# Performance work log

Hardware: AMD Instinct MI355X
Metric: run time of the kernel (lower is better)

The kernel has to match this reference:

```python
import jax, jax.numpy as jnp
import numpy as np

B, S, E, A = 4, 4096, 512, 64

def setup_inputs() -> dict:
    key = jax.random.key(0)
    ks = jax.random.split(key, 9)
    return {
        "query": jax.random.normal(ks[0], (B, S, E), dtype=jnp.float32),
        "key":   jax.random.normal(ks[1], (B, S, E), dtype=jnp.float32),
        "value": jax.random.normal(ks[2], (B, S, E), dtype=jnp.float32),
        "Wq": jax.random.normal(ks[3], (E, A), dtype=jnp.float32) / np.sqrt(E),
        "bq": jax.random.normal(ks[4], (A,), dtype=jnp.float32) * 0.01,
        "Wk": jax.random.normal(ks[5], (E, A), dtype=jnp.float32) / np.sqrt(E),
        "bk": jax.random.normal(ks[6], (A,), dtype=jnp.float32) * 0.01,
        "Wv": jax.random.normal(ks[7], (E, A), dtype=jnp.float32) / np.sqrt(E),
        "bv": jax.random.normal(ks[8], (A,), dtype=jnp.float32) * 0.01,
        "look_ahead_mask": 1,
    }

def reference(query, key, value, Wq, bq, Wk, bk, Wv, bv, look_ahead_mask):
    # Linear projections (torch Linear: x @ W^T + b; here W stored as [in,out])
    q = query @ Wq + bq            # [B,S,A]
    k = key   @ Wk + bk            # [B,S,A]
    v = value @ Wv + bv            # [B,S,A]
    scale = jnp.sqrt(jnp.asarray(A, dtype=q.dtype))
    qk = jnp.einsum('bsa,bta->bst', q, k) / scale   # [B,S,S]
    if look_ahead_mask:
        # faithful to source: MULTIPLICATIVE tril mask (not additive -inf)
        tril = jnp.tril(jnp.ones((qk.shape[-1], qk.shape[-1]), dtype=qk.dtype))
        qk = qk * tril
    attn = jax.nn.softmax(qk, axis=-1)              # [B,S,S]
    return jnp.einsum('bst,bta->bsa', attn, v)       # [B,S,A]
```

## Files before the change

### kernel.cpp

```cpp
#include <hip/hip_runtime.h>
#include <cstdint>

constexpr int BB = 4, SS = 4096, EE = 512, AA = 64;
constexpr int NT = 64;
constexpr int NSL = 288;

typedef __bf16 bf16x8 __attribute__((ext_vector_type(8)));
typedef float  f32x4  __attribute__((ext_vector_type(4)));
typedef float  f4     __attribute__((ext_vector_type(4)));
typedef unsigned short u16x4 __attribute__((ext_vector_type(4)));
typedef unsigned short u16x8 __attribute__((ext_vector_type(8)));

#define MFMA16(a, b, c) __builtin_amdgcn_mfma_f32_16x16x32_bf16((a), (b), (c), 0, 0, 0)

typedef const void __attribute__((address_space(1))) gvoid_t;
typedef void __attribute__((address_space(3))) lvoid_t;
__device__ __forceinline__ void gload16(const void* g, void* l) {
    __builtin_amdgcn_global_load_lds((gvoid_t*)g, (lvoid_t*)l, 16, 0, 0);
}

__device__ __forceinline__ unsigned short f2bf(float x) {
    union { float f; unsigned u; } v; v.f = x;
    unsigned r = v.u + 0x7fffu + ((v.u >> 16) & 1u);
    return (unsigned short)(r >> 16);
}
__device__ __forceinline__ float bf2f(unsigned short h) {
    union { unsigned u; float f; } v; v.u = ((unsigned)h) << 16;
    return v.f;
}
__device__ __forceinline__ bf16x8 as_bf16x8(u16x8 u) {
    union { u16x8 u; bf16x8 b; } v; v.u = u; return v.b;
}

__global__ void split_w_kernel(const float* __restrict__ Wq,
                               const float* __restrict__ Wk,
                               const float* __restrict__ Wv,
                               unsigned short* __restrict__ wt_h,
                               unsigned short* __restrict__ wt_l) {
    int idx = blockIdx.x * blockDim.x + threadIdx.x;
    if (idx >= 3 * EE * AA) return;
    int t = idx / (EE * AA);
    int rem = idx - t * (EE * AA);
    int k = rem >> 6;
    int n = rem & 63;
    const float* W = (t == 0) ? Wq : (t == 1) ? Wk : Wv;
    float x = W[k * AA + n];
    unsigned short h = f2bf(x);
    unsigned short l = f2bf(x - bf2f(h));
    int o = (t * AA + n) * EE + k;
    wt_h[o] = h;
    wt_l[o] = l;
}

__launch_bounds__(256)
__global__ void proj_kernel(const float* __restrict__ Xq,
                            const float* __restrict__ Xk,
                            const float* __restrict__ Xv,
                            const float* __restrict__ bq,
                            const float* __restrict__ bk,
                            const float* __restrict__ bv,
                            const unsigned short* __restrict__ wt_h,
                            const unsigned short* __restrict__ wt_l,
                            unsigned short* __restrict__ q_hi,
                            unsigned short* __restrict__ q_lo,
                            unsigned short* __restrict__ kv) {
    const int t = blockIdx.y;
    const float* X    = (t == 0) ? Xq : (t == 1) ? Xk : Xv;
    const float* bias = (t == 0) ? bq : (t == 1) ? bk : bv;
    const int row0 = blockIdx.x * 64;
    const int tid = threadIdx.x;
    const int lane = tid & 63, w = tid >> 6;
    const int l15 = lane & 15, l4 = lane >> 4;

    __shared__ __align__(16) char smem[32768];

    f32x4 acc[4];
#pragma unroll
    for (int j = 0; j < 4; ++j) acc[j] = (f32x4){0.f, 0.f, 0.f, 0.f};

    const unsigned short* wtH = wt_h + t * AA * EE;
    const unsigned short* wtL = wt_l + t * AA * EE;

    for (int kc0 = 0; kc0 < EE; kc0 += 64) {
#pragma unroll
        for (int s = 0; s < 4; ++s) {
            int r = w * 16 + s * 4 + (lane >> 4);
            int c4 = (lane & 15) ^ (r & 7);
            gload16(X + (size_t)(row0 + r) * EE + kc0 + c4 * 4,
                    smem + w * 4096 + s * 1024 + lane * 16);
        }
#pragma unroll
        for (int s = 0; s < 2; ++s) {
            int n = w * 16 + s * 8 + (lane >> 3);
            int cg = (lane & 7) ^ (n & 7);
            gload16(wtH + n * EE + kc0 + cg * 8,
                    smem + 16384 + w * 2048 + s * 1024 + lane * 16);
            gload16(wtL + n * EE + kc0 + cg * 8,
                    smem + 24576 + w * 2048 + s * 1024 + lane * 16);
        }
        asm volatile("s_waitcnt vmcnt(0)" ::: "memory");
        __syncthreads();

#pragma unroll
        for (int kc = 0; kc < 2; ++kc) {
            int r = w * 16 + l15;
            int c4a = (kc * 8 + l4 * 2) ^ (r & 7);
            int c4b = (kc * 8 + l4 * 2 + 1) ^ (r & 7);
            f4 va = *(const f4*)(smem + r * 256 + c4a * 16);
            f4 vb = *(const f4*)(smem + r * 256 + c4b * 16);
            u16x8 ahu, alu;
#pragma unroll
            for (int jj = 0; jj < 4; ++jj) {
                unsigned short h0 = f2bf(va[jj]);
                ahu[jj] = h0;
                alu[jj] = f2bf(va[jj] - bf2f(h0));
                unsigned short h1 = f2bf(vb[jj]);
                ahu[jj + 4] = h1;
                alu[jj + 4] = f2bf(vb[jj] - bf2f(h1));
            }
            bf16x8 a_h = as_bf16x8(ahu), a_l = as_bf16x8(alu);
#pragma unroll
            for (int j = 0; j < 4; ++j) {
                int n = j * 16 + l15;
                int byteB = n * 128 + (((kc * 4 + l4) ^ (n & 7)) << 4);
                bf16x8 b_h = as_bf16x8(*(const u16x8*)(smem + 16384 + byteB));
                bf16x8 b_l = as_bf16x8(*(const u16x8*)(smem + 24576 + byteB));
                acc[j] = MFMA16(a_h, b_h, acc[j]);
                acc[j] = MFMA16(a_h, b_l, acc[j]);
                acc[j] = MFMA16(a_l, b_h, acc[j]);
            }
        }
        __syncthreads();
    }

    float* stage = (float*)smem;
#pragma unroll
    for (int j = 0; j < 4; ++j) {
        int n = j * 16 + l15;
        float bv_ = bias[n];
#pragma unroll
        for (int reg = 0; reg < 4; ++reg) {
            int r = w * 16 + l4 * 4 + reg;
            stage[r * 65 + n] = acc[j][reg] + bv_;
        }
    }
    __syncthreads();

    if (t == 0) {
        int row = tid >> 2, n0 = (tid & 3) * 16;
        u16x8 h0, l0, h1, l1;
#pragma unroll
        for (int k = 0; k < 8; ++k) {
            float v = stage[row * 65 + n0 + k];
            unsigned short hh = f2bf(v);
            h0[k] = hh; l0[k] = f2bf(v - bf2f(hh));
        }
#pragma unroll
        for (int k = 0; k < 8; ++k) {
            float v = stage[row * 65 + n0 + 8 + k];
            unsigned short hh = f2bf(v);
            h1[k] = hh; l1[k] = f2bf(v - bf2f(hh));
        }
        size_t o = (size_t)(row0 + row) * AA + n0;
        *(u16x8*)(q_hi + o) = h0; *(u16x8*)(q_hi + o + 8) = h1;
        *(u16x8*)(q_lo + o) = l0; *(u16x8*)(q_lo + o + 8) = l1;
    } else {
        const int bb = row0 >> 12, kt = (row0 & 4095) >> 6;
        const size_t base = ((size_t)(bb * NT + kt) << 14) + (t == 2 ? 8192 : 0);
        const int f = tid >> 5;
#pragma unroll
        for (int p = 0; p < 2; ++p) {
            int lane2 = (tid & 31) * 2 + p;
            u16x8 h, l;
            if (t == 1) {
                int n0 = (f >> 2) * 32 + (lane2 >> 4) * 8;
                int tt = (f & 3) * 16 + (lane2 & 15);
#pragma unroll
                for (int jj = 0; jj < 8; ++jj) {
                    float v = stage[tt * 65 + n0 + jj];
                    unsigned short hh = f2bf(v);
                    h[jj] = hh; l[jj] = f2bf(v - bf2f(hh));
                }
            } else {
                int tt0 = (f >> 2) * 32 + (lane2 >> 4) * 8;
                int n = (f & 3) * 16 + (lane2 & 15);
#pragma unroll
                for (int jj = 0; jj < 8; ++jj) {
                    float v = stage[(tt0 + jj) * 65 + n];
                    unsigned short hh = f2bf(v);
                    h[jj] = hh; l[jj] = f2bf(v - bf2f(hh));
                }
            }
            size_t o = base + f * 512 + lane2 * 8;
            *(u16x8*)(kv + o) = h;
            *(u16x8*)(kv + o + 4096) = l;
        }
    }
}

__launch_bounds__(64)
__global__ void sufv_kernel(const unsigned short* __restrict__ kv,
                            float* __restrict__ sufv) {
    const int b = blockIdx.x >> 6;
    const int a = blockIdx.x & 63;
    const int t = threadIdx.x;
    __shared__ float sums[64];
    const size_t tb = ((size_t)(b * NT + t) << 14) + 8192;
    const int j = a >> 4, l15i = a & 15;
    float s = 0.f;
#pragma unroll
    for (int c2 = 0; c2 < 2; ++c2) {
#pragma unroll
        for (int l4i = 0; l4i < 4; ++l4i) {
            size_t off = tb + (((c2 * 4 + j) * 64 + l4i * 16 + l15i) << 3);
            u16x8 h = *(const u16x8*)(kv + off);
            u16x8 l = *(const u16x8*)(kv + off + 4096);
#pragma unroll
            for (int q = 0; q < 8; ++q) s += bf2f(h[q]) + bf2f(l[q]);
        }
    }
    sums[t] = s;
    __syncthreads();
    float suf = 0.f;
    for (int jj = t + 1; jj < 64; ++jj) suf += sums[jj];
    sufv[((size_t)(b * 64 + a)) * 64 + t] = suf;
}

__launch_bounds__(256)
__global__ void attn_chunk_kernel(const unsigned short* __restrict__ q_hi,
                                  const unsigned short* __restrict__ q_lo,
                                  const unsigned short* __restrict__ kv,
                                  float* __restrict__ facc_part,
                                  float* __restrict__ l_part) {
    const int bxr = (NSL - 1) - blockIdx.x;
    const int b = blockIdx.y;
    int g = 7;
    while (4 * g * (g + 1) > bxr) --g;
    const int r_ = bxr - 4 * g * (g + 1);
    const int q_ = (int)((float)r_ * (1.0f / (float)(g + 1)) + 1e-4f);
    const int i  = g * 8 + q_;
    const int c  = r_ - q_ * (g + 1);
    const int t_begin = c * 8;
    const int t_end   = (t_begin + 8 < i + 1) ? t_begin + 8 : i + 1;

    const int tid = threadIdx.x;
    const int lane = tid & 63, w = tid >> 6;
    const int l15 = lane & 15, l4 = lane >> 4;

    __shared__ __align__(16) unsigned short kvbuf[16384];
    __shared__ __align__(16) unsigned short plds[4][1024];

    bf16x8 qh[2], ql[2];
    {
        size_t qrow = (size_t)(b * SS + i * 64 + w * 16 + l15) * AA;
#pragma unroll
        for (int kc = 0; kc < 2; ++kc) {
            qh[kc] = as_bf16x8(*(const u16x8*)(q_hi + qrow + kc * 32 + l4 * 8));
            ql[kc] = as_bf16x8(*(const u16x8*)(q_lo + qrow + kc * 32 + l4 * 8));
        }
    }

    f32x4 facc[4];
#pragma unroll
    for (int j = 0; j < 4; ++j) facc[j] = (f32x4){0.f, 0.f, 0.f, 0.f};
    float lsum[4] = {0.f, 0.f, 0.f, 0.f};

    const char* lb = (const char*)kvbuf;

    for (int kt = t_begin; kt < t_end; ++kt) {
        {
            const char* gt = (const char*)kv + (((size_t)(b * NT + kt)) << 15) +
                             w * 8192 + lane * 16;
            char* lw = (char*)kvbuf + w * 8192;
#pragma unroll
            for (int s = 0; s < 8; ++s) gload16(gt + s * 1024, lw + s * 1024);
        }
        asm volatile("s_waitcnt vmcnt(0)" ::: "memory");
        __syncthreads();

        f32x4 sc[4];
#pragma unroll
        for (int j = 0; j < 4; ++j) sc[j] = (f32x4){0.f, 0.f, 0.f, 0.f};
#pragma unroll
        for (int kc = 0; kc < 2; ++kc) {
#pragma unroll
            for (int j2 = 0; j2 < 4; ++j2) {
                int f = kc * 4 + j2;
                bf16x8 h = as_bf16x8(*(const u16x8*)(lb + f * 1024 + lane * 16));
                bf16x8 l = as_bf16x8(*(const u16x8*)(lb + 8192 + f * 1024 + lane * 16));
                sc[j2] = MFMA16(qh[kc], h, sc[j2]);
                sc[j2] = MFMA16(qh[kc], l, sc[j2]);
                sc[j2] = MFMA16(ql[kc], h, sc[j2]);
            }
        }

        const bool diag = (kt == i);
        float pv[4][4];
#pragma unroll
        for (int j2 = 0; j2 < 4; ++j2) {
#pragma unroll
            for (int reg = 0; reg < 4; ++reg) {
                float s = sc[j2][reg] * 0.125f;
                if (diag) {
                    int qr = w * 16 + l4 * 4 + reg;
                    int tg = j2 * 16 + l15;
                    if (tg > qr) s = 0.f;
                }
                float p = __expf(s);
                pv[j2][reg] = p;
                lsum[reg] += p;
            }
        }
#pragma unroll
        for (int j2 = 0; j2 < 4; ++j2) {
#pragma unroll
            for (int reg = 0; reg < 4; ++reg) {
                int row = l4 * 4 + reg, col = j2 * 16 + l15;
                int byte = (row * 128 + col * 2) ^ ((row & 7) << 4);
                *(unsigned short*)((char*)plds[w] + byte) = f2bf(pv[j2][reg]);
            }
        }
#pragma unroll
        for (int c2 = 0; c2 < 2; ++c2) {
            int byteA = (l15 * 128 + c2 * 64 + l4 * 16) ^ ((l15 & 7) << 4);
            bf16x8 pf = as_bf16x8(*(const u16x8*)((const char*)plds[w] + byteA));
#pragma unroll
            for (int j = 0; j < 4; ++j) {
                int f = c2 * 4 + j;
                bf16x8 vh = as_bf16x8(*(const u16x8*)(lb + 16384 + f * 1024 + lane * 16));
                bf16x8 vl = as_bf16x8(*(const u16x8*)(lb + 24576 + f * 1024 + lane * 16));
                facc[j] = MFMA16(pf, vh, facc[j]);
                facc[j] = MFMA16(pf, vl, facc[j]);
            }
        }
        __syncthreads();
    }

#pragma unroll
    for (int reg = 0; reg < 4; ++reg) {
        float rs = lsum[reg];
#pragma unroll
        for (int off = 1; off < 16; off <<= 1) rs += __shfl_xor(rs, off);
        lsum[reg] = rs;
    }

    const size_t slot = (size_t)b * NSL + bxr;
    float* fp = facc_part + slot * 4096;
#pragma unroll
    for (int j = 0; j < 4; ++j) {
#pragma unroll
        for (int reg = 0; reg < 4; ++reg) {
            int row = w * 16 + l4 * 4 + reg, a = j * 16 + l15;
            fp[row * 64 + a] = facc[j][reg];
        }
    }
    if (l15 == 0) {
#pragma unroll
        for (int reg = 0; reg < 4; ++reg)
            l_part[slot * 64 + w * 16 + l4 * 4 + reg] = lsum[reg];
    }
}

__launch_bounds__(256)
__global__ void combine_kernel(const float* __restrict__ facc_part,
                               const float* __restrict__ l_part,
                               const float* __restrict__ sufv,
                               float* __restrict__ out) {
    const int i = blockIdx.x;
    const int b = blockIdx.y;
    const int tid = threadIdx.x;
    const int g = i >> 3;
    const int nch = g + 1;
    const size_t slot0 = (size_t)b * NSL + 4 * g * (g + 1) + (i & 7) * nch;
    __shared__ float linv[64];
    __shared__ float sv[64];
    if (tid < 64) {
        float l = (float)(64 * (NT - 1 - i));
        for (int cc = 0; cc < nch; ++cc) l += l_part[(slot0 + cc) * 64 + tid];
        linv[tid] = 1.f / l;
        sv[tid] = sufv[((size_t)(b * 64 + tid)) * 64 + i];
    }
    __syncthreads();
    float* ob = out + ((size_t)(b * SS + i * 64)) * AA;
#pragma unroll
    for (int k = 0; k < 4; ++k) {
        int e = (tid + k * 256) * 4;
        int row = e >> 6, a = e & 63;
        f4 acc = {sv[a], sv[a + 1], sv[a + 2], sv[a + 3]};
        for (int cc = 0; cc < nch; ++cc) {
            f4 v = *(const f4*)(facc_part + (slot0 + cc) * 4096 + e);
            acc += v;
        }
        acc *= linv[row];
        *(f4*)(ob + e) = acc;
    }
}

extern "C" void kernel_launch(void* const* d_in, const int* in_sizes, int n_in,
                              void* d_out, int out_size, void* d_ws, size_t ws_size,
                              hipStream_t stream) {
    const float* query = (const float*)d_in[0];
    const float* key   = (const float*)d_in[1];
    const float* value = (const float*)d_in[2];
    const float* Wq    = (const float*)d_in[3];
    const float* bq    = (const float*)d_in[4];
    const float* Wk    = (const float*)d_in[5];
    const float* bk    = (const float*)d_in[6];
    const float* Wv    = (const float*)d_in[7];
    const float* bv    = (const float*)d_in[8];

    char* ws = (char*)d_ws;
    const size_t MB = 1u << 20;
    unsigned short* q_hi = (unsigned short*)(ws + 0 * MB);
    unsigned short* q_lo = (unsigned short*)(ws + 2 * MB);
    unsigned short* kv   = (unsigned short*)(ws + 4 * MB);
    float* sufv      = (float*)(ws + 12 * MB);
    float* l_part    = (float*)(ws + 13 * MB);
    float* facc_part = (float*)(ws + 14 * MB);
    unsigned short* wt_h = (unsigned short*)(ws + 34 * MB);
    unsigned short* wt_l = wt_h + 3 * AA * EE;

    split_w_kernel<<<(3 * EE * AA + 255) / 256, 256, 0, stream>>>(Wq, Wk, Wv, wt_h, wt_l);
    proj_kernel<<<dim3(BB * SS / 64, 3), 256, 0, stream>>>(
        query, key, value, bq, bk, bv, wt_h, wt_l, q_hi, q_lo, kv);
    sufv_kernel<<<BB * AA, 64, 0, stream>>>(kv, sufv);
    attn_chunk_kernel<<<dim3(NSL, BB), 256, 0, stream>>>(
        q_hi, q_lo, kv, facc_part, l_part);
    combine_kernel<<<dim3(NT, BB), 256, 0, stream>>>(facc_part, l_part, sufv, (float*)d_out);
}
```

Baseline: 90.49 us.

## Prefetch next KV tile into registers and transpose QK MFMA operands

Replaces the synchronous global_load_lds of each KV tile with a register prefetch of the next tile, issued before the current tile's compute and stored to LDS after it, so global load latency overlaps the MFMA work. Swaps the QK^T MFMA operand order so each lane holds four consecutive key columns of one query row. This lets P be written to LDS as packed 4-element stores and the row sum be reduced with two shuffles instead of four. It also adds s_setprio around the MFMA sections. The cost is 8 extra vector registers per lane and a second barrier per iteration.

```diff
diff --git a/kernel.cpp b/kernel.cpp
--- a/kernel.cpp
+++ b/kernel.cpp
@@ -263,24 +263,37 @@
     f32x4 facc[4];
 #pragma unroll
     for (int j = 0; j < 4; ++j) facc[j] = (f32x4){0.f, 0.f, 0.f, 0.f};
-    float lsum[4] = {0.f, 0.f, 0.f, 0.f};
-
+    float lsum = 0.f;
+
+    const char* gbase_p = (const char*)kv + (((size_t)(b * NT)) << 15) +
+                          w * 8192 + lane * 16;
+    char* lw = (char*)kvbuf + w * 8192 + lane * 16;
     const char* lb = (const char*)kvbuf;
 
+    f4 rr[8];
+
+    {
+        const char* gt = gbase_p + (((size_t)t_begin) << 15);
+#pragma unroll
+        for (int s = 0; s < 8; ++s) rr[s] = *(const f4*)(gt + s * 1024);
+#pragma unroll
+        for (int s = 0; s < 8; ++s) *(f4*)(lw + s * 1024) = rr[s];
+    }
+    __syncthreads();
+
     for (int kt = t_begin; kt < t_end; ++kt) {
-        {
-            const char* gt = (const char*)kv + (((size_t)(b * NT + kt)) << 15) +
-                             w * 8192 + lane * 16;
-            char* lw = (char*)kvbuf + w * 8192;
-#pragma unroll
-            for (int s = 0; s < 8; ++s) gload16(gt + s * 1024, lw + s * 1024);
-        }
-        asm volatile("s_waitcnt vmcnt(0)" ::: "memory");
-        __syncthreads();
+        const bool more = (kt + 1 < t_end);
+        if (more) {
+            const char* gt = gbase_p + (((size_t)(kt + 1)) << 15);
+#pragma unroll
+            for (int s = 0; s < 8; ++s) rr[s] = *(const f4*)(gt + s * 1024);
+        }
+        __builtin_amdgcn_sched_barrier(0);
 
         f32x4 sc[4];
 #pragma unroll
         for (int j = 0; j < 4; ++j) sc[j] = (f32x4){0.f, 0.f, 0.f, 0.f};
+        __builtin_amdgcn_s_setprio(1);
 #pragma unroll
         for (int kc = 0; kc < 2; ++kc) {
 #pragma unroll
@@ -288,38 +301,34 @@
                 int f = kc * 4 + j2;
                 bf16x8 h = as_bf16x8(*(const u16x8*)(lb + f * 1024 + lane * 16));
                 bf16x8 l = as_bf16x8(*(const u16x8*)(lb + 8192 + f * 1024 + lane * 16));
-                sc[j2] = MFMA16(qh[kc], h, sc[j2]);
-                sc[j2] = MFMA16(qh[kc], l, sc[j2]);
-                sc[j2] = MFMA16(ql[kc], h, sc[j2]);
-            }
-        }
+                sc[j2] = MFMA16(h, qh[kc], sc[j2]);
+                sc[j2] = MFMA16(l, qh[kc], sc[j2]);
+                sc[j2] = MFMA16(h, ql[kc], sc[j2]);
+            }
+        }
+        __builtin_amdgcn_s_setprio(0);
 
         const bool diag = (kt == i);
-        float pv[4][4];
 #pragma unroll
         for (int j2 = 0; j2 < 4; ++j2) {
+            u16x4 p4;
 #pragma unroll
             for (int reg = 0; reg < 4; ++reg) {
                 float s = sc[j2][reg] * 0.125f;
                 if (diag) {
-                    int qr = w * 16 + l4 * 4 + reg;
-                    int tg = j2 * 16 + l15;
+                    int qr = w * 16 + l15;
+                    int tg = j2 * 16 + l4 * 4 + reg;
                     if (tg > qr) s = 0.f;
                 }
                 float p = __expf(s);
-                pv[j2][reg] = p;
-                lsum[reg] += p;
-            }
-        }
-#pragma unroll
-        for (int j2 = 0; j2 < 4; ++j2) {
-#pragma unroll
-            for (int reg = 0; reg < 4; ++reg) {
-                int row = l4 * 4 + reg, col = j2 * 16 + l15;
-                int byte = (row * 128 + col * 2) ^ ((row & 7) << 4);
-                *(unsigned short*)((char*)plds[w] + byte) = f2bf(pv[j2][reg]);
-            }
-        }
+                lsum += p;
+                p4[reg] = f2bf(p);
+            }
+            int byte = (l15 * 128 + j2 * 32 + l4 * 8) ^ ((l15 & 7) << 4);
+            *(u16x4*)((char*)plds[w] + byte) = p4;
+        }
+
+        __builtin_amdgcn_s_setprio(1);
 #pragma unroll
         for (int c2 = 0; c2 < 2; ++c2) {
             int byteA = (l15 * 128 + c2 * 64 + l4 * 16) ^ ((l15 & 7) << 4);
@@ -333,31 +342,33 @@
                 facc[j] = MFMA16(pf, vl, facc[j]);
             }
         }
-        __syncthreads();
-    }
-
-#pragma unroll
-    for (int reg = 0; reg < 4; ++reg) {
-        float rs = lsum[reg];
-#pragma unroll
-        for (int off = 1; off < 16; off <<= 1) rs += __shfl_xor(rs, off);
-        lsum[reg] = rs;
-    }
-
-    const size_t slot = (size_t)b * NSL + bxr;
-    float* fp = facc_part + slot * 4096;
-#pragma unroll
-    for (int j = 0; j < 4; ++j) {
-#pragma unroll
-        for (int reg = 0; reg < 4; ++reg) {
-            int row = w * 16 + l4 * 4 + reg, a = j * 16 + l15;
-            fp[row * 64 + a] = facc[j][reg];
-        }
-    }
-    if (l15 == 0) {
-#pragma unroll
-        for (int reg = 0; reg < 4; ++reg)
-            l_part[slot * 64 + w * 16 + l4 * 4 + reg] = lsum[reg];
+        __builtin_amdgcn_s_setprio(0);
+
+        if (more) {
+            __syncthreads();
+#pragma unroll
+            for (int s = 0; s < 8; ++s) *(f4*)(lw + s * 1024) = rr[s];
+            __syncthreads();
+        }
+    }
+
+    {
+        float rs = lsum;
+        rs += __shfl_xor(rs, 16);
+        rs += __shfl_xor(rs, 32);
+        const size_t slot = (size_t)b * NSL + bxr;
+        if (l4 == 0)
+            l_part[slot * 64 + w * 16 + l15] = rs;
+
+        float* fp = facc_part + slot * 4096;
+#pragma unroll
+        for (int j = 0; j < 4; ++j) {
+#pragma unroll
+            for (int reg = 0; reg < 4; ++reg) {
+                int row = w * 16 + l4 * 4 + reg, a = j * 16 + l15;
+                fp[row * 64 + a] = facc[j][reg];
+            }
+        }
     }
 }
 
```

New measurement: 90.32 us. No clear change (-0.2%).
